# Performance work log

Hardware: AMD Instinct MI355X
Metric: run time of the kernel (lower is better)

The kernel has to match this reference:

```python
import jax, jax.numpy as jnp
import numpy as np

B = 16          # graphs per batch
NN = 2000       # nodes per graph (num_nodes)
N = B * NN      # total nodes in the batched graph
F_IN = 128      # input node features
H, C = 4, 64    # heads, per-head out channels (both GAT layers)
HC = H * C
DEG = 12        # average degree per node
FC1, FC2, OUT = 512, 128, 1
FC_IN = 6 * NN  # len(which_layer) = 6


def setup_inputs() -> dict:
    key = jax.random.key(0)
    ks = jax.random.split(key, 32)

    def g(i, shape, s=0.05):
        return jax.random.normal(ks[i], shape, jnp.float32) * s

    # within-graph random edges, no self loops (GATConv removes then re-adds them)
    src_l = jax.random.randint(ks[0], (B, NN * DEG), 0, NN)
    off = jax.random.randint(ks[1], (B, NN * DEG), 1, NN)
    dst_l = (src_l + off) % NN
    goff = (jnp.arange(B) * NN)[:, None]
    edge_index = jnp.stack([(src_l + goff).reshape(-1),
                            (dst_l + goff).reshape(-1)]).astype(jnp.int32)

    return {
        "x": g(2, (N, F_IN), 1.0),
        "W1": g(3, (F_IN, HC)), "att_src1": g(4, (H, C)), "att_dst1": g(5, (H, C)),
        "b1": jnp.zeros((HC,), jnp.float32),
        "W2": g(6, (HC, HC)), "att_src2": g(7, (H, C)), "att_dst2": g(8, (H, C)),
        "b2": jnp.zeros((HC,), jnp.float32),
        "pw1": g(9, (HC, 1)), "pb1": jnp.zeros((1,), jnp.float32),
        "pw2": g(10, (HC, 1)), "pb2": jnp.zeros((1,), jnp.float32),
        "ln_w": jnp.ones((NN,), jnp.float32), "ln_b": jnp.zeros((NN,), jnp.float32),
        "sex_emb": g(11, (2, NN)), "mut_emb": g(12, (4, NN)),
        "age_w": g(13, (NN,)), "age_b": jnp.zeros((NN,), jnp.float32),
        "fw1": g(14, (FC_IN, FC1)), "fb1": jnp.zeros((FC1,), jnp.float32),
        "fw2": g(15, (FC1, FC2)), "fb2": jnp.zeros((FC2,), jnp.float32),
        "fw3": g(16, (FC2, OUT)), "fb3": jnp.zeros((OUT,), jnp.float32),
        "age": jax.random.uniform(ks[17], (B,), jnp.float32),
        "edge_index": edge_index,
        "sex": jax.random.randint(ks[18], (B,), 0, 2),
        "mutation": jax.random.randint(ks[19], (B,), 0, 4),
    }


def _layer_norm(x, w, b, eps=1e-5):
    mu = jnp.mean(x, -1, keepdims=True)
    var = jnp.mean((x - mu) ** 2, -1, keepdims=True)
    return (x - mu) / jnp.sqrt(var + eps) * w + b


def _gat_conv(x, W, att_src, att_dst, bias, src, dst):
    h = (x @ W).reshape(N, H, C)                         # [N,H,C]
    a_s = jnp.sum(h * att_src[None], -1)                 # [N,H]
    a_d = jnp.sum(h * att_dst[None], -1)                 # [N,H]
    alpha = jax.nn.leaky_relu(a_s[src] + a_d[dst], 0.2)  # [E,H]
    m = jax.ops.segment_max(alpha, dst, num_segments=N)  # segment softmax over dst
    e = jnp.exp(alpha - m[dst])
    denom = jax.ops.segment_sum(e, dst, num_segments=N)
    a = e / (denom[dst] + 1e-16)
    out = jax.ops.segment_sum(a[:, :, None] * h[src], dst, num_segments=N)
    return out.reshape(N, HC) + bias


def _forward(x, W1, att_src1, att_dst1, b1, W2, att_src2, att_dst2, b2,
             pw1, pb1, pw2, pb2, ln_w, ln_b, sex_emb, mut_emb, age_w, age_b,
             fw1, fb1, fw2, fb2, fw3, fb3, age, edge_index, sex, mutation):
    loop = jnp.arange(N, dtype=edge_index.dtype)         # self loops added by GATConv
    src = jnp.concatenate([edge_index[0], loop])
    dst = jnp.concatenate([edge_index[1], loop])

    x0 = jnp.mean(x, -1).reshape(B, NN)                  # to_dense_batch(mean(x,-1))

    h = jax.nn.relu(_gat_conv(x, W1, att_src1, att_dst1, b1, src, dst))
    x1 = (h @ pw1 + pb1).squeeze(-1).reshape(B, NN)
    h = jax.nn.relu(_gat_conv(h, W2, att_src2, att_dst2, b2, src, dst))
    x2 = (h @ pw2 + pb2).squeeze(-1).reshape(B, NN)

    x0 = _layer_norm(x0, ln_w, ln_b)
    x1 = _layer_norm(x1, ln_w, ln_b)
    x2 = _layer_norm(x2, ln_w, ln_b)
    ms = jnp.concatenate([x0, x1, x2], axis=1)           # [B, 3*NN]

    demo = jnp.concatenate([sex_emb[sex], mut_emb[mutation],
                            age[:, None] * age_w[None, :] + age_b], axis=1)
    t = jnp.concatenate([demo, ms], axis=1)              # [B, 6*NN]
    t = jax.nn.relu(t @ fw1 + fb1)
    t = jax.nn.relu(t @ fw2 + fb2)
    pred = t @ fw3 + fb3                                 # [B, 1]
    return pred, x0, x1, x2, ms


def reference(x, W1, att_src1, att_dst1, b1, W2, att_src2, att_dst2, b2,
              pw1, pb1, pw2, pb2, ln_w, ln_b, sex_emb, mut_emb, age_w, age_b,
              fw1, fb1, fw2, fb2, fw3, fb3, age, edge_index, sex, mutation):
    return _forward(x, W1, att_src1, att_dst1, b1, W2, att_src2, att_dst2, b2,
                    pw1, pb1, pw2, pb2, ln_w, ln_b, sex_emb, mut_emb, age_w, age_b,
                    fw1, fb1, fw2, fb2, fw3, fb3, age, edge_index, sex, mutation)
```

## Files before the change

### kernel.cpp

```cpp
#include <hip/hip_runtime.h>
#include <math.h>

#define NTOT   32000
#define NNODE  2000
#define NB     16
#define FIN    128
#define HCDIM  256
#define NH     4
#define FC1DIM 512
#define FC2DIM 128
#define FCIN   12000
#define KC1    50
#define NCH1   240
#define CAP    64
#define BK     32
#define LPITCH 40

typedef __attribute__((ext_vector_type(8))) short bf16x8;
typedef __attribute__((ext_vector_type(4))) float f32x4;

__device__ inline float4 ld4(const float* p){ return *reinterpret_cast<const float4*>(p); }
__device__ inline void st4(float* p, float4 v){ *reinterpret_cast<float4*>(p) = v; }
__device__ inline float4 add4(float4 a, float4 b){ return make_float4(a.x+b.x,a.y+b.y,a.z+b.z,a.w+b.w); }
__device__ inline float4 max4(float4 a, float4 b){ return make_float4(fmaxf(a.x,b.x),fmaxf(a.y,b.y),fmaxf(a.z,b.z),fmaxf(a.w,b.w)); }
__device__ inline float lrelu(float x){ return x > 0.f ? x : 0.2f*x; }
__device__ inline float4 leaky4(float4 a){ return make_float4(lrelu(a.x),lrelu(a.y),lrelu(a.z),lrelu(a.w)); }
__device__ inline float4 exp4s(float4 a, float4 m){ return make_float4(__expf(a.x-m.x),__expf(a.y-m.y),__expf(a.z-m.z),__expf(a.w-m.w)); }
__device__ inline float dot4(float4 a, float4 b){ return a.x*b.x + a.y*b.y + a.z*b.z + a.w*b.w; }
__device__ inline float selh(float4 v, int h){ return h==0 ? v.x : (h==1 ? v.y : (h==2 ? v.z : v.w)); }

__device__ inline unsigned short f2bf(float f){
  unsigned int u = __float_as_uint(f);
  u += 0x7FFFu + ((u >> 16) & 1u);
  return (unsigned short)(u >> 16);
}
__device__ inline float bf2f(unsigned short h){
  return __uint_as_float(((unsigned int)h) << 16);
}
__device__ inline float4 ldbf4(const unsigned short* p){
  ushort4 v = *reinterpret_cast<const ushort4*>(p);
  return make_float4(bf2f(v.x), bf2f(v.y), bf2f(v.z), bf2f(v.w));
}

__device__ inline float4 redmax4_64(float4 m){
  #pragma unroll
  for(int off=1; off<64; off<<=1){
    m.x = fmaxf(m.x, __shfl_xor(m.x, off));
    m.y = fmaxf(m.y, __shfl_xor(m.y, off));
    m.z = fmaxf(m.z, __shfl_xor(m.z, off));
    m.w = fmaxf(m.w, __shfl_xor(m.w, off));
  }
  return m;
}
__device__ inline float4 redsum4_64(float4 d){
  #pragma unroll
  for(int off=1; off<64; off<<=1){
    d.x += __shfl_xor(d.x, off);
    d.y += __shfl_xor(d.y, off);
    d.z += __shfl_xor(d.z, off);
    d.w += __shfl_xor(d.w, off);
  }
  return d;
}

__global__ void k_zero(int* p, int n){
  int i = blockIdx.x*blockDim.x + threadIdx.x;
  if(i < n) p[i] = 0;
}

__global__ void k_build(const int* __restrict__ src, const int* __restrict__ dst,
                        int* __restrict__ cnt, int* __restrict__ col, int e0){
  int i = blockIdx.x*blockDim.x + threadIdx.x;
  if(i < e0){
    int d = dst[i];
    int slot = atomicAdd(&cnt[d], 1);
    if(slot < CAP) col[(d<<6) + slot] = src[i];
  }
}

__global__ __launch_bounds__(256) void k_prep(const float* __restrict__ x,
                                              unsigned short* __restrict__ xb,
                                              float* __restrict__ x0r){
  int lane = threadIdx.x & 63, wv = threadIdx.x >> 6;
  int n = blockIdx.x*4 + wv;
  const float* r = x + (size_t)n*FIN;
  float2 v = *reinterpret_cast<const float2*>(r + lane*2);
  unsigned int packed = (unsigned int)f2bf(v.x) | ((unsigned int)f2bf(v.y) << 16);
  *reinterpret_cast<unsigned int*>(xb + (size_t)n*FIN + lane*2) = packed;
  float s = v.x + v.y;
  #pragma unroll
  for(int off=1; off<64; off<<=1) s += __shfl_xor(s, off);
  if(lane == 0) x0r[n] = s * (1.0f/FIN);
}

__global__ void k_tr(const float* __restrict__ W, unsigned short* __restrict__ Wt,
                     int K, int N){
  int idx = blockIdx.x*blockDim.x + threadIdx.x;
  if(idx < N*K){
    int n = idx / K, k = idx - n*K;
    Wt[idx] = f2bf(W[(size_t)k*N + n]);
  }
}

__global__ __launch_bounds__(256) void k_gemm_bf(const unsigned short* __restrict__ A,
                                                 const unsigned short* __restrict__ Bt,
                                                 unsigned short* __restrict__ C,
                                                 int M, int K){
  __shared__ unsigned short As[128][LPITCH];
  __shared__ unsigned short Bs[128][LPITCH];
  int tid = threadIdx.x;
  int lane = tid & 63, wv = tid >> 6;
  int wm = (wv & 1)*64, wn = (wv >> 1)*64;
  int m0 = blockIdx.y*128, n0 = blockIdx.x*128;
  int l15 = lane & 15, lq = lane >> 4;
  f32x4 acc[4][4];
  #pragma unroll
  for(int i=0;i<4;i++)
    #pragma unroll
    for(int j=0;j<4;j++)
      acc[i][j] = (f32x4){0.f,0.f,0.f,0.f};

  int r = tid >> 2, c = (tid & 3)*8;
  for(int k0 = 0; k0 < K; k0 += BK){
    *reinterpret_cast<uint4*>(&As[r][c])    = *reinterpret_cast<const uint4*>(A  + (size_t)(m0+r)*K + k0 + c);
    *reinterpret_cast<uint4*>(&As[r+64][c]) = *reinterpret_cast<const uint4*>(A  + (size_t)(m0+r+64)*K + k0 + c);
    *reinterpret_cast<uint4*>(&Bs[r][c])    = *reinterpret_cast<const uint4*>(Bt + (size_t)(n0+r)*K + k0 + c);
    *reinterpret_cast<uint4*>(&Bs[r+64][c]) = *reinterpret_cast<const uint4*>(Bt + (size_t)(n0+r+64)*K + k0 + c);
    __syncthreads();
    bf16x8 af[4], bf[4];
    #pragma unroll
    for(int i=0;i<4;i++){
      af[i] = *reinterpret_cast<const bf16x8*>(&As[wm + i*16 + l15][lq*8]);
      bf[i] = *reinterpret_cast<const bf16x8*>(&Bs[wn + i*16 + l15][lq*8]);
    }
    #pragma unroll
    for(int mi=0;mi<4;mi++)
      #pragma unroll
      for(int ni=0;ni<4;ni++)
        acc[mi][ni] = __builtin_amdgcn_mfma_f32_16x16x32_bf16(af[mi], bf[ni], acc[mi][ni], 0, 0, 0);
    __syncthreads();
  }
  #pragma unroll
  for(int mi=0;mi<4;mi++){
    #pragma unroll
    for(int ni=0;ni<4;ni++){
      int cn = n0 + wn + ni*16 + l15;
      #pragma unroll
      for(int rg=0;rg<4;rg++){
        int rm = m0 + wm + mi*16 + lq*4 + rg;
        C[(size_t)rm*HCDIM + cn] = f2bf(acc[mi][ni][rg]);
      }
    }
  }
}

__global__ __launch_bounds__(256) void k_attn(const unsigned short* __restrict__ hpre,
                                              const float* __restrict__ attS,
                                              const float* __restrict__ attD,
                                              float* __restrict__ a_s,
                                              float* __restrict__ a_d){
  int lane = threadIdx.x & 63;
  int n = blockIdx.x*4 + (threadIdx.x >> 6);
  int f0 = lane*4;
  float4 hv = ldbf4(hpre + (size_t)n*HCDIM + f0);
  float4 sv = ld4(attS + f0);
  float4 dv = ld4(attD + f0);
  float ps = dot4(hv, sv), pd = dot4(hv, dv);
  #pragma unroll
  for(int off=1; off<16; off<<=1){ ps += __shfl_xor(ps, off); pd += __shfl_xor(pd, off); }
  if((lane & 15) == 0){
    int h = lane >> 4;
    a_s[n*4+h] = ps; a_d[n*4+h] = pd;
  }
}

template<int STORE>
__global__ __launch_bounds__(256) void k_agg(const unsigned short* __restrict__ hpre,
                                             const float* __restrict__ a_s,
                                             const float* __restrict__ a_d,
                                             const int* __restrict__ cnt,
                                             const int* __restrict__ col,
                                             const float* __restrict__ bias,
                                             const float* __restrict__ pw,
                                             const float* __restrict__ pb,
                                             unsigned short* __restrict__ hout,
                                             float* __restrict__ xraw){
  __shared__ float4 ew[4][CAP];
  int tid = threadIdx.x;
  int lane = tid & 63, wv = tid >> 6;
  int blk  = blockIdx.x;
  int xcd  = blk & 7;
  int slot = blk >> 3;
  int half = slot / 500;
  int g    = xcd + 8*half;
  int n    = g*NNODE + (slot - half*500)*4 + wv;
  int f0 = lane*4;
  int hl = lane >> 4;
  float4 ad   = ld4(a_d + n*4);
  float4 asn  = ld4(a_s + n*4);
  float4 aself = leaky4(add4(asn, ad));
  float4 m = aself;
  int deg = min(cnt[n], CAP);
  int base = n << 6;
  if(lane < deg){
    int s = col[base + lane];
    m = max4(m, leaky4(add4(ld4(a_s + s*4), ad)));
  }
  m = redmax4_64(m);
  float4 d;
  if(lane < deg){
    int s = col[base + lane];
    float4 al = leaky4(add4(ld4(a_s + s*4), ad));
    float4 ex = exp4s(al, m);
    ew[wv][lane] = ex;
    d = ex;
  } else {
    d = make_float4(0.f,0.f,0.f,0.f);
  }
  if(lane == 0) d = add4(d, exp4s(aself, m));
  d = redsum4_64(d);
  float invh = 1.0f / (selh(d, hl) + 1e-16f);
  float wself = __expf(selh(aself, hl) - selh(m, hl)) * invh;
  float4 hv = ldbf4(hpre + (size_t)n*HCDIM + f0);
  float4 acc = make_float4(wself*hv.x, wself*hv.y, wself*hv.z, wself*hv.w);
  __syncthreads();
  const float* ewf = (const float*)&ew[wv][0];
  for(int e = 0; e < deg; e++){
    int s = col[base + e];
    float w = ewf[e*4 + hl] * invh;
    float4 h2 = ldbf4(hpre + (size_t)s*HCDIM + f0);
    acc.x = fmaf(w, h2.x, acc.x); acc.y = fmaf(w, h2.y, acc.y);
    acc.z = fmaf(w, h2.z, acc.z); acc.w = fmaf(w, h2.w, acc.w);
  }
  float4 b4 = ld4(bias + f0);
  acc = make_float4(fmaxf(acc.x+b4.x,0.f), fmaxf(acc.y+b4.y,0.f),
                    fmaxf(acc.z+b4.z,0.f), fmaxf(acc.w+b4.w,0.f));
  if(STORE){
    ushort4 hb = make_ushort4(f2bf(acc.x), f2bf(acc.y), f2bf(acc.z), f2bf(acc.w));
    *reinterpret_cast<ushort4*>(hout + (size_t)n*HCDIM + f0) = hb;
  }
  float part = dot4(acc, ld4(pw + f0));
  #pragma unroll
  for(int off=1; off<64; off<<=1) part += __shfl_xor(part, off);
  if(lane == 0) xraw[n] = part + pb[0];
}

__global__ __launch_bounds__(256) void k_ln(const float* __restrict__ xraw,
                                            const float* __restrict__ lnw,
                                            const float* __restrict__ lnb,
                                            float* __restrict__ out,
                                            float* __restrict__ t, int which){
  int b = blockIdx.x;
  const float* src = xraw + b*NNODE;
  __shared__ float red[8];
  int tid = threadIdx.x, lane = tid & 63, wv = tid >> 6;
  float s = 0.f, ss = 0.f;
  for(int i = tid; i < NNODE; i += 256){ float v = src[i]; s += v; ss += v*v; }
  #pragma unroll
  for(int off=1; off<64; off<<=1){ s += __shfl_xor(s, off); ss += __shfl_xor(ss, off); }
  if(lane == 0){ red[wv] = s; red[4+wv] = ss; }
  __syncthreads();
  s  = red[0]+red[1]+red[2]+red[3];
  ss = red[4]+red[5]+red[6]+red[7];
  float mu  = s * (1.0f/NNODE);
  float var = ss * (1.0f/NNODE) - mu*mu;
  float inv = 1.0f / sqrtf(var + 1e-5f);
  float* o1 = out + 16 + which*(NB*NNODE) + b*NNODE;
  float* o2 = out + 16 + 3*(NB*NNODE) + b*(3*NNODE) + which*NNODE;
  float* o3 = t + b*FCIN + 3*NNODE + which*NNODE;
  for(int i = tid; i < NNODE; i += 256){
    float v = (src[i]-mu)*inv*lnw[i] + lnb[i];
    o1[i] = v; o2[i] = v; o3[i] = v;
  }
}

__global__ void k_demo(const float* __restrict__ sexemb, const float* __restrict__ mutemb,
                       const float* __restrict__ agew, const float* __restrict__ ageb,
                       const float* __restrict__ age, const int* __restrict__ sex,
                       const int* __restrict__ mut, float* __restrict__ t){
  int i = blockIdx.x*blockDim.x + threadIdx.x;
  int b = i / (3*NNODE);
  int j = i - b*(3*NNODE);
  float v;
  if(j < NNODE)          v = sexemb[sex[b]*NNODE + j];
  else if(j < 2*NNODE)   v = mutemb[mut[b]*NNODE + (j - NNODE)];
  else                   v = age[b]*agew[j - 2*NNODE] + ageb[j - 2*NNODE];
  t[b*FCIN + j] = v;
}

__global__ __launch_bounds__(256) void k_fc1p(const float* __restrict__ t,
                                              const float* __restrict__ fw1,
                                              float* __restrict__ partial){
  __shared__ float ts[NB][KC1];
  __shared__ float red[NB][FC1DIM];
  int tid = threadIdx.x;
  int half = tid >> 7;
  int c4 = (tid & 127) * 4;
  int k0 = blockIdx.x * KC1;
  for(int i = tid; i < NB*KC1; i += 256){
    int b = i / KC1, kk = i - b*KC1;
    ts[b][kk] = t[b*FCIN + k0 + kk];
  }
  __syncthreads();
  float4 acc[NB];
  #pragma unroll
  for(int b=0;b<NB;b++) acc[b] = make_float4(0.f,0.f,0.f,0.f);
  for(int kk = half; kk < KC1; kk += 2){
    float4 w = ld4(fw1 + (size_t)(k0+kk)*FC1DIM + c4);
    #pragma unroll
    for(int b=0;b<NB;b++){
      float tv = ts[b][kk];
      acc[b].x = fmaf(tv, w.x, acc[b].x);
      acc[b].y = fmaf(tv, w.y, acc[b].y);
      acc[b].z = fmaf(tv, w.z, acc[b].z);
      acc[b].w = fmaf(tv, w.w, acc[b].w);
    }
  }
  if(half == 1){
    #pragma unroll
    for(int b=0;b<NB;b++) st4(&red[b][c4], acc[b]);
  }
  __syncthreads();
  if(half == 0){
    float* po = partial + (size_t)blockIdx.x*(NB*FC1DIM);
    #pragma unroll
    for(int b=0;b<NB;b++){
      float4 r = ld4(&red[b][c4]);
      st4(po + b*FC1DIM + c4, add4(acc[b], r));
    }
  }
}

__global__ void k_fc1r(const float* __restrict__ partial, const float* __restrict__ fb1,
                       float* __restrict__ t1){
  int i = blockIdx.x*blockDim.x + threadIdx.x;
  float s = fb1[i & (FC1DIM-1)];
  for(int c=0;c<NCH1;c++) s += partial[(size_t)c*(NB*FC1DIM) + i];
  t1[i] = fmaxf(s, 0.f);
}

__global__ void k_fc2(const float* __restrict__ t1, const float* __restrict__ fw2,
                      const float* __restrict__ fb2, float* __restrict__ t2){
  int i = blockIdx.x*blockDim.x + threadIdx.x;
  int b = i >> 7, j = i & 127;
  float s = fb2[j];
  for(int k=0;k<FC1DIM;k++) s = fmaf(t1[b*FC1DIM+k], fw2[k*FC2DIM+j], s);
  t2[i] = fmaxf(s, 0.f);
}

__global__ void k_fc3(const float* __restrict__ t2, const float* __restrict__ fw3,
                      const float* __restrict__ fb3, float* __restrict__ pred){
  int b = blockIdx.x;
  int lane = threadIdx.x;
  float s = t2[b*FC2DIM + lane]*fw3[lane] + t2[b*FC2DIM + 64 + lane]*fw3[64 + lane];
  #pragma unroll
  for(int off=1; off<64; off<<=1) s += __shfl_xor(s, off);
  if(lane == 0) pred[b] = s + fb3[0];
}

extern "C" void kernel_launch(void* const* d_in, const int* in_sizes, int n_in,
                              void* d_out, int out_size, void* d_ws, size_t ws_size,
                              hipStream_t stream) {
  const float* x       = (const float*)d_in[0];
  const float* W1      = (const float*)d_in[1];
  const float* attS1   = (const float*)d_in[2];
  const float* attD1   = (const float*)d_in[3];
  const float* b1      = (const float*)d_in[4];
  const float* W2      = (const float*)d_in[5];
  const float* attS2   = (const float*)d_in[6];
  const float* attD2   = (const float*)d_in[7];
  const float* b2      = (const float*)d_in[8];
  const float* pw1     = (const float*)d_in[9];
  const float* pb1     = (const float*)d_in[10];
  const float* pw2     = (const float*)d_in[11];
  const float* pb2     = (const float*)d_in[12];
  const float* lnw     = (const float*)d_in[13];
  const float* lnb     = (const float*)d_in[14];
  const float* sexemb  = (const float*)d_in[15];
  const float* mutemb  = (const float*)d_in[16];
  const float* agew    = (const float*)d_in[17];
  const float* ageb    = (const float*)d_in[18];
  const float* fw1     = (const float*)d_in[19];
  const float* fb1     = (const float*)d_in[20];
  const float* fw2     = (const float*)d_in[21];
  const float* fb2     = (const float*)d_in[22];
  const float* fw3     = (const float*)d_in[23];
  const float* fb3     = (const float*)d_in[24];
  const float* age     = (const float*)d_in[25];
  const int*   eidx    = (const int*)d_in[26];
  const int*   sex     = (const int*)d_in[27];
  const int*   mut     = (const int*)d_in[28];
  const int E0 = in_sizes[26] / 2;
  const int* esrc = eidx;
  const int* edst = eidx + E0;

  float* out = (float*)d_out;

  float* w = (float*)d_ws;
  float* a_s  = w;
  float* a_d  = a_s + NTOT*NH;
  float* x0r  = a_d + NTOT*NH;
  float* x1r  = x0r + NTOT;
  float* x2r  = x1r + NTOT;
  float* tbuf = x2r + NTOT;
  float* part = tbuf + NB*FCIN;
  float* t1   = part + (size_t)NCH1*NB*FC1DIM;
  float* t2   = t1 + NB*FC1DIM;
  unsigned short* xb  = (unsigned short*)(t2 + NB*FC2DIM);
  unsigned short* hA  = xb  + (size_t)NTOT*FIN;
  unsigned short* hB  = hA  + (size_t)NTOT*HCDIM;
  unsigned short* W1t = hB  + (size_t)NTOT*HCDIM;
  unsigned short* W2t = W1t + HCDIM*FIN;
  int* cnt    = (int*)(W2t + HCDIM*HCDIM);
  int* col    = cnt + NTOT;
  (void)ws_size; (void)n_in; (void)out_size;

  const int eb = (E0 + 255)/256;

  k_zero<<<(NTOT+255)/256, 256, 0, stream>>>(cnt, NTOT);
  k_build<<<eb, 256, 0, stream>>>(esrc, edst, cnt, col, E0);
  k_prep<<<NTOT/4, 256, 0, stream>>>(x, xb, x0r);
  k_tr<<<(HCDIM*FIN+255)/256, 256, 0, stream>>>(W1, W1t, FIN, HCDIM);
  k_tr<<<(HCDIM*HCDIM+255)/256, 256, 0, stream>>>(W2, W2t, HCDIM, HCDIM);

  k_gemm_bf<<<dim3(HCDIM/128, NTOT/128), 256, 0, stream>>>(xb, W1t, hA, NTOT, FIN);
  k_attn<<<NTOT/4, 256, 0, stream>>>(hA, attS1, attD1, a_s, a_d);
  k_agg<1><<<NTOT/4, 256, 0, stream>>>(hA, a_s, a_d, cnt, col, b1, pw1, pb1, hB, x1r);

  k_gemm_bf<<<dim3(HCDIM/128, NTOT/128), 256, 0, stream>>>(hB, W2t, hA, NTOT, HCDIM);
  k_attn<<<NTOT/4, 256, 0, stream>>>(hA, attS2, attD2, a_s, a_d);
  k_agg<0><<<NTOT/4, 256, 0, stream>>>(hA, a_s, a_d, cnt, col, b2, pw2, pb2, hB, x2r);

  k_demo<<<(NB*3*NNODE)/256, 256, 0, stream>>>(sexemb, mutemb, agew, ageb, age, sex, mut, tbuf);
  k_ln<<<NB, 256, 0, stream>>>(x0r, lnw, lnb, out, tbuf, 0);
  k_ln<<<NB, 256, 0, stream>>>(x1r, lnw, lnb, out, tbuf, 1);
  k_ln<<<NB, 256, 0, stream>>>(x2r, lnw, lnb, out, tbuf, 2);

  k_fc1p<<<NCH1, 256, 0, stream>>>(tbuf, fw1, part);
  k_fc1r<<<(NB*FC1DIM)/256, 256, 0, stream>>>(part, fb1, t1);
  k_fc2<<<(NB*FC2DIM)/256, 256, 0, stream>>>(t1, fw2, fb2, t2);
  k_fc3<<<NB, 64, 0, stream>>>(t2, fw3, fb3, out);
}
```

Before: 322.4 us.

## Fuse attention logits into GEMM epilogue and merge small launches

```diff
diff --git a/kernel.cpp b/kernel.cpp
--- a/kernel.cpp
+++ b/kernel.cpp
@@ -63,9 +63,22 @@
   return d;
 }
 
-__global__ void k_zero(int* p, int n){
-  int i = blockIdx.x*blockDim.x + threadIdx.x;
-  if(i < n) p[i] = 0;
+__global__ __launch_bounds__(256) void k_prep(const float* __restrict__ x,
+                                              unsigned short* __restrict__ xb,
+                                              float* __restrict__ x0r,
+                                              int* __restrict__ cnt){
+  int gid = blockIdx.x*256 + threadIdx.x;
+  if(gid < NTOT) cnt[gid] = 0;
+  int lane = threadIdx.x & 63, wv = threadIdx.x >> 6;
+  int n = blockIdx.x*4 + wv;
+  const float* r = x + (size_t)n*FIN;
+  float2 v = *reinterpret_cast<const float2*>(r + lane*2);
+  unsigned int packed = (unsigned int)f2bf(v.x) | ((unsigned int)f2bf(v.y) << 16);
+  *reinterpret_cast<unsigned int*>(xb + (size_t)n*FIN + lane*2) = packed;
+  float s = v.x + v.y;
+  #pragma unroll
+  for(int off=1; off<64; off<<=1) s += __shfl_xor(s, off);
+  if(lane == 0) x0r[n] = s * (1.0f/FIN);
 }
 
 __global__ void k_build(const int* __restrict__ src, const int* __restrict__ dst,
@@ -78,33 +91,26 @@
   }
 }
 
-__global__ __launch_bounds__(256) void k_prep(const float* __restrict__ x,
-                                              unsigned short* __restrict__ xb,
-                                              float* __restrict__ x0r){
-  int lane = threadIdx.x & 63, wv = threadIdx.x >> 6;
-  int n = blockIdx.x*4 + wv;
-  const float* r = x + (size_t)n*FIN;
-  float2 v = *reinterpret_cast<const float2*>(r + lane*2);
-  unsigned int packed = (unsigned int)f2bf(v.x) | ((unsigned int)f2bf(v.y) << 16);
-  *reinterpret_cast<unsigned int*>(xb + (size_t)n*FIN + lane*2) = packed;
-  float s = v.x + v.y;
-  #pragma unroll
-  for(int off=1; off<64; off<<=1) s += __shfl_xor(s, off);
-  if(lane == 0) x0r[n] = s * (1.0f/FIN);
-}
-
-__global__ void k_tr(const float* __restrict__ W, unsigned short* __restrict__ Wt,
-                     int K, int N){
+__global__ void k_tr2(const float* __restrict__ W1, const float* __restrict__ W2,
+                      unsigned short* __restrict__ W1t, unsigned short* __restrict__ W2t){
   int idx = blockIdx.x*blockDim.x + threadIdx.x;
-  if(idx < N*K){
-    int n = idx / K, k = idx - n*K;
-    Wt[idx] = f2bf(W[(size_t)k*N + n]);
+  if(idx < HCDIM*FIN){
+    int n = idx / FIN, k = idx - n*FIN;
+    W1t[idx] = f2bf(W1[(size_t)k*HCDIM + n]);
+  } else {
+    int j = idx - HCDIM*FIN;
+    int n = j / HCDIM, k = j - n*HCDIM;
+    W2t[j] = f2bf(W2[(size_t)k*HCDIM + n]);
   }
 }
 
 __global__ __launch_bounds__(256) void k_gemm_bf(const unsigned short* __restrict__ A,
                                                  const unsigned short* __restrict__ Bt,
                                                  unsigned short* __restrict__ C,
+                                                 const float* __restrict__ attS,
+                                                 const float* __restrict__ attD,
+                                                 float* __restrict__ a_s,
+                                                 float* __restrict__ a_d,
                                                  int M, int K){
   __shared__ unsigned short As[128][LPITCH];
   __shared__ unsigned short Bs[128][LPITCH];
@@ -127,17 +133,17 @@
     *reinterpret_cast<uint4*>(&Bs[r][c])    = *reinterpret_cast<const uint4*>(Bt + (size_t)(n0+r)*K + k0 + c);
     *reinterpret_cast<uint4*>(&Bs[r+64][c]) = *reinterpret_cast<const uint4*>(Bt + (size_t)(n0+r+64)*K + k0 + c);
     __syncthreads();
-    bf16x8 af[4], bf[4];
+    bf16x8 af[4], bfr[4];
     #pragma unroll
     for(int i=0;i<4;i++){
-      af[i] = *reinterpret_cast<const bf16x8*>(&As[wm + i*16 + l15][lq*8]);
-      bf[i] = *reinterpret_cast<const bf16x8*>(&Bs[wn + i*16 + l15][lq*8]);
+      af[i]  = *reinterpret_cast<const bf16x8*>(&As[wm + i*16 + l15][lq*8]);
+      bfr[i] = *reinterpret_cast<const bf16x8*>(&Bs[wn + i*16 + l15][lq*8]);
     }
     #pragma unroll
     for(int mi=0;mi<4;mi++)
       #pragma unroll
       for(int ni=0;ni<4;ni++)
-        acc[mi][ni] = __builtin_amdgcn_mfma_f32_16x16x32_bf16(af[mi], bf[ni], acc[mi][ni], 0, 0, 0);
+        acc[mi][ni] = __builtin_amdgcn_mfma_f32_16x16x32_bf16(af[mi], bfr[ni], acc[mi][ni], 0, 0, 0);
     __syncthreads();
   }
   #pragma unroll
@@ -152,25 +158,36 @@
       }
     }
   }
-}
-
-__global__ __launch_bounds__(256) void k_attn(const unsigned short* __restrict__ hpre,
-                                              const float* __restrict__ attS,
-                                              const float* __restrict__ attD,
-                                              float* __restrict__ a_s,
-                                              float* __restrict__ a_d){
-  int lane = threadIdx.x & 63;
-  int n = blockIdx.x*4 + (threadIdx.x >> 6);
-  int f0 = lane*4;
-  float4 hv = ldbf4(hpre + (size_t)n*HCDIM + f0);
-  float4 sv = ld4(attS + f0);
-  float4 dv = ld4(attD + f0);
-  float ps = dot4(hv, sv), pd = dot4(hv, dv);
-  #pragma unroll
-  for(int off=1; off<16; off<<=1){ ps += __shfl_xor(ps, off); pd += __shfl_xor(pd, off); }
-  if((lane & 15) == 0){
-    int h = lane >> 4;
-    a_s[n*4+h] = ps; a_d[n*4+h] = pd;
+  int head = (n0 + wn) >> 6;
+  float avs[4], avd[4];
+  #pragma unroll
+  for(int ni=0;ni<4;ni++){
+    int cc = ni*16 + l15;
+    avs[ni] = attS[head*64 + cc];
+    avd[ni] = attD[head*64 + cc];
+  }
+  #pragma unroll
+  for(int mi=0;mi<4;mi++){
+    #pragma unroll
+    for(int rg=0;rg<4;rg++){
+      float ps = 0.f, pd = 0.f;
+      #pragma unroll
+      for(int ni=0;ni<4;ni++){
+        float v = acc[mi][ni][rg];
+        ps = fmaf(avs[ni], v, ps);
+        pd = fmaf(avd[ni], v, pd);
+      }
+      #pragma unroll
+      for(int off=1; off<16; off<<=1){
+        ps += __shfl_xor(ps, off);
+        pd += __shfl_xor(pd, off);
+      }
+      if(l15 == 0){
+        int rm = m0 + wm + mi*16 + lq*4 + rg;
+        a_s[rm*4 + head] = ps;
+        a_d[rm*4 + head] = pd;
+      }
+    }
   }
 }
 
@@ -245,13 +262,14 @@
   if(lane == 0) xraw[n] = part + pb[0];
 }
 
-__global__ __launch_bounds__(256) void k_ln(const float* __restrict__ xraw,
-                                            const float* __restrict__ lnw,
-                                            const float* __restrict__ lnb,
-                                            float* __restrict__ out,
-                                            float* __restrict__ t, int which){
-  int b = blockIdx.x;
-  const float* src = xraw + b*NNODE;
+__global__ __launch_bounds__(256) void k_ln3(const float* __restrict__ xraw0,
+                                             const float* __restrict__ lnw,
+                                             const float* __restrict__ lnb,
+                                             float* __restrict__ out,
+                                             float* __restrict__ t){
+  int blk = blockIdx.x;
+  int b = blk & 15, which = blk >> 4;
+  const float* src = xraw0 + which*NTOT + b*NNODE;
   __shared__ float red[8];
   int tid = threadIdx.x, lane = tid & 63, wv = tid >> 6;
   float s = 0.f, ss = 0.f;
@@ -339,23 +357,24 @@
   t1[i] = fmaxf(s, 0.f);
 }
 
-__global__ void k_fc2(const float* __restrict__ t1, const float* __restrict__ fw2,
-                      const float* __restrict__ fb2, float* __restrict__ t2){
-  int i = blockIdx.x*blockDim.x + threadIdx.x;
-  int b = i >> 7, j = i & 127;
+__global__ __launch_bounds__(128) void k_head2(const float* __restrict__ t1,
+                                               const float* __restrict__ fw2,
+                                               const float* __restrict__ fb2,
+                                               const float* __restrict__ fw3,
+                                               const float* __restrict__ fb3,
+                                               float* __restrict__ pred){
+  __shared__ float red[2];
+  int b = blockIdx.x, j = threadIdx.x;
+  const float* tr = t1 + b*FC1DIM;
   float s = fb2[j];
-  for(int k=0;k<FC1DIM;k++) s = fmaf(t1[b*FC1DIM+k], fw2[k*FC2DIM+j], s);
-  t2[i] = fmaxf(s, 0.f);
-}
-
-__global__ void k_fc3(const float* __restrict__ t2, const float* __restrict__ fw3,
-                      const float* __restrict__ fb3, float* __restrict__ pred){
-  int b = blockIdx.x;
-  int lane = threadIdx.x;
-  float s = t2[b*FC2DIM + lane]*fw3[lane] + t2[b*FC2DIM + 64 + lane]*fw3[64 + lane];
+  for(int k=0;k<FC1DIM;k++) s = fmaf(tr[k], fw2[k*FC2DIM+j], s);
+  s = fmaxf(s, 0.f) * fw3[j];
   #pragma unroll
   for(int off=1; off<64; off<<=1) s += __shfl_xor(s, off);
-  if(lane == 0) pred[b] = s + fb3[0];
+  int lane = j & 63, wv = j >> 6;
+  if(lane == 0) red[wv] = s;
+  __syncthreads();
+  if(j == 0) pred[b] = red[0] + red[1] + fb3[0];
 }
 
 extern "C" void kernel_launch(void* const* d_in, const int* in_sizes, int n_in,
@@ -405,8 +424,7 @@
   float* tbuf = x2r + NTOT;
   float* part = tbuf + NB*FCIN;
   float* t1   = part + (size_t)NCH1*NB*FC1DIM;
-  float* t2   = t1 + NB*FC1DIM;
-  unsigned short* xb  = (unsigned short*)(t2 + NB*FC2DIM);
+  unsigned short* xb  = (unsigned short*)(t1 + NB*FC1DIM);
   unsigned short* hA  = xb  + (size_t)NTOT*FIN;
   unsigned short* hB  = hA  + (size_t)NTOT*HCDIM;
   unsigned short* W1t = hB  + (size_t)NTOT*HCDIM;
@@ -417,27 +435,20 @@
 
   const int eb = (E0 + 255)/256;
 
-  k_zero<<<(NTOT+255)/256, 256, 0, stream>>>(cnt, NTOT);
+  k_prep<<<NTOT/4, 256, 0, stream>>>(x, xb, x0r, cnt);
   k_build<<<eb, 256, 0, stream>>>(esrc, edst, cnt, col, E0);
-  k_prep<<<NTOT/4, 256, 0, stream>>>(x, xb, x0r);
-  k_tr<<<(HCDIM*FIN+255)/256, 256, 0, stream>>>(W1, W1t, FIN, HCDIM);
-  k_tr<<<(HCDIM*HCDIM+255)/256, 256, 0, stream>>>(W2, W2t, HCDIM, HCDIM);
-
-  k_gemm_bf<<<dim3(HCDIM/128, NTOT/128), 256, 0, stream>>>(xb, W1t, hA, NTOT, FIN);
-  k_attn<<<NTOT/4, 256, 0, stream>>>(hA, attS1, attD1, a_s, a_d);
+  k_tr2<<<(HCDIM*FIN + HCDIM*HCDIM)/256, 256, 0, stream>>>(W1, W2, W1t, W2t);
+
+  k_gemm_bf<<<dim3(HCDIM/128, NTOT/128), 256, 0, stream>>>(xb, W1t, hA, attS1, attD1, a_s, a_d, NTOT, FIN);
   k_agg<1><<<NTOT/4, 256, 0, stream>>>(hA, a_s, a_d, cnt, col, b1, pw1, pb1, hB, x1r);
 
-  k_gemm_bf<<<dim3(HCDIM/128, NTOT/128), 256, 0, stream>>>(hB, W2t, hA, NTOT, HCDIM);
-  k_attn<<<NTOT/4, 256, 0, stream>>>(hA, attS2, attD2, a_s, a_d);
+  k_gemm_bf<<<dim3(HCDIM/128, NTOT/128), 256, 0, stream>>>(hB, W2t, hA, attS2, attD2, a_s, a_d, NTOT, HCDIM);
   k_agg<0><<<NTOT/4, 256, 0, stream>>>(hA, a_s, a_d, cnt, col, b2, pw2, pb2, hB, x2r);
 
   k_demo<<<(NB*3*NNODE)/256, 256, 0, stream>>>(sexemb, mutemb, agew, ageb, age, sex, mut, tbuf);
-  k_ln<<<NB, 256, 0, stream>>>(x0r, lnw, lnb, out, tbuf, 0);
-  k_ln<<<NB, 256, 0, stream>>>(x1r, lnw, lnb, out, tbuf, 1);
-  k_ln<<<NB, 256, 0, stream>>>(x2r, lnw, lnb, out, tbuf, 2);
+  k_ln3<<<3*NB, 256, 0, stream>>>(x0r, lnw, lnb, out, tbuf);
 
   k_fc1p<<<NCH1, 256, 0, stream>>>(tbuf, fw1, part);
   k_fc1r<<<(NB*FC1DIM)/256, 256, 0, stream>>>(part, fb1, t1);
-  k_fc2<<<(NB*FC2DIM)/256, 256, 0, stream>>>(t1, fw2, fb2, t2);
-  k_fc3<<<NB, 64, 0, stream>>>(t2, fw3, fb3, out);
-}
+  k_head2<<<NB, 128, 0, stream>>>(t1, fw2, fb2, fw3, fb3, out);
+}
```

Result: faster. 292.1 us (-9.4%).
